# Optimization experiments

Measured on AMD Instinct MI355X. Metric: run time of the kernel, lower is better.

## Reference

```python
import jax, jax.numpy as jnp
import numpy as np

NG, N, NFG, NFR, NFP, B = 4, 64, 1024, 256, 256, 2048
SCALE = 1.0 / float(np.sqrt(NFR + NFP))
EPS = 1e-5  # torch LayerNorm default


def setup_inputs() -> dict:
    key = jax.random.key(0)
    k = jax.random.split(key, 4)
    x = jax.random.normal(k[0], (B, N, NFG), dtype=jnp.float32)
    # per-graph params stacked over NG for vectorized computation
    Wt = jax.random.normal(k[1], (NG, NFR, NFG), dtype=jnp.float32) * 0.02
    bt = jnp.zeros((NG, NFR), dtype=jnp.float32)
    Wp = jax.random.normal(k[2], (NG, NFR, NFG), dtype=jnp.float32) * 0.02
    bp = jnp.zeros((NG, NFR), dtype=jnp.float32)
    Wg = jax.random.normal(k[3], (NG, NFG, NFG), dtype=jnp.float32) * 0.02  # [out,in]
    gamma = jnp.ones((NG, NFG), dtype=jnp.float32)
    beta = jnp.zeros((NG, NFG), dtype=jnp.float32)
    return {"x": x, "Wt": Wt, "bt": bt, "Wp": Wp, "bp": bp,
            "Wg": Wg, "gamma": gamma, "beta": beta}


def reference(x, Wt, bt, Wp, bp, Wg, gamma, beta):
    # theta/phi projections, vectorized over NG graphs: [G,B,N,R]
    theta = jnp.einsum('bnf,grf->gbnr', x, Wt) + bt[:, None, None, :]
    phi = jnp.einsum('bnf,grf->gbnr', x, Wp) + bp[:, None, None, :]
    # original computes sim=theta@phi^T then .sum(2); identical math:
    # relation[b,n] = theta[b,n] . sum_m phi[b,m]  (avoids the NxN matrix)
    phi_sum = phi.sum(axis=2)                                  # [G,B,R]
    relation = jnp.einsum('gbnr,gbr->gbn', theta, phi_sum) * SCALE
    w = jax.nn.softmax(relation, axis=2)                       # softmax over boxes N
    # attention-weighted aggregation over boxes -> [G,B,NFG]
    agg = jnp.einsum('gbn,bnf->gbf', w, x)
    # GCN linear (no bias): [G,B,NFG]
    h = jnp.einsum('gbf,gof->gbo', agg, Wg)
    # LayerNorm over feature dim, per graph
    mu = h.mean(axis=-1, keepdims=True)
    var = ((h - mu) ** 2).mean(axis=-1, keepdims=True)
    h = (h - mu) * jax.lax.rsqrt(var + EPS) * gamma[:, None, :] + beta[:, None, :]
    h = jax.nn.relu(h)
    # mean over the NG graphs; restore keepdim axis -> [B,1,NFG]
    return h.mean(axis=0)[:, None, :]
```

## Files before the change

kernel.cpp:

```cpp
#include <hip/hip_runtime.h>
#include <hip/hip_bf16.h>

typedef __attribute__((ext_vector_type(4))) float f4;
typedef __attribute__((ext_vector_type(4))) float f32x4;
typedef __attribute__((ext_vector_type(8))) short short8;
typedef __attribute__((ext_vector_type(2))) unsigned int u32x2;
typedef __attribute__((ext_vector_type(4))) unsigned int u32x4;
typedef unsigned int u32;
typedef unsigned short u16;

#define SCALE_F 0.04419417382415922f

__device__ inline u16 f2bf(float f) {
  u32 u = __float_as_uint(f);
  u32 r = u + 0x7FFFu + ((u >> 16) & 1u);
  return (u16)(r >> 16);
}
__device__ inline u32 pk(float a, float b) {
  return (u32)f2bf(a) | ((u32)f2bf(b) << 16);
}
__device__ inline float bflo(u32 u) { return __uint_as_float(u << 16); }
__device__ inline float bfhi(u32 u) { return __uint_as_float(u & 0xFFFF0000u); }

#define GLD16(gsrc, ldst)                                                     \
  __builtin_amdgcn_global_load_lds(                                           \
      (const __attribute__((address_space(1))) void*)(gsrc),                  \
      (__attribute__((address_space(3))) void*)(ldst), 16, 0, 0)

#define SWZ(o) (((o) & ~2047) | (((((o) >> 4) & 127) ^ (((o) >> 11) & 7)) << 4))

__device__ __forceinline__ void cvt8(const float* __restrict__ src,
                                     u16* __restrict__ dst, int blk, int t) {
  int i = blk * 256 + t;
  const f4* s = (const f4*)src;
  f4 a = s[(size_t)i * 2];
  f4 b = s[(size_t)i * 2 + 1];
  u32x4 p;
  p[0] = pk(a[0], a[1]);
  p[1] = pk(a[2], a[3]);
  p[2] = pk(b[0], b[1]);
  p[3] = pk(b[2], b[3]);
  *(u32x4*)(dst + (size_t)i * 8) = p;
}

__global__ __launch_bounds__(256) void k01_prep(const float* __restrict__ x,
                                                const float* __restrict__ Wg,
                                                const float* __restrict__ Wp,
                                                const float* __restrict__ Wt,
                                                u16* __restrict__ xs16,
                                                char* __restrict__ xpre,
                                                u16* __restrict__ wgb,
                                                u16* __restrict__ wpb,
                                                u16* __restrict__ wtb) {
  __shared__ float red[256][8];
  __shared__ u16 tile[64][66];
  const int blk = blockIdx.x, t = threadIdx.x;
  if (blk < 2048) {
    const int b = blk;
    const float* xb = x + (size_t)b * 65536;
    char* xp = xpre + (size_t)b * 131072;
    const int g16 = t & 127, rp = t >> 7;
    f4 acc0 = {0.f, 0.f, 0.f, 0.f}, acc1 = {0.f, 0.f, 0.f, 0.f};
#pragma unroll 8
    for (int it = 0; it < 32; ++it) {
      int n = it * 2 + rp;
      const float* src = xb + n * 1024 + g16 * 8;
      f4 v0 = *(const f4*)(src);
      f4 v1 = *(const f4*)(src + 4);
      acc0 += v0;
      acc1 += v1;
      u32x4 p;
      p[0] = pk(v0[0], v0[1]);
      p[1] = pk(v0[2], v0[3]);
      p[2] = pk(v1[0], v1[1]);
      p[3] = pk(v1[2], v1[3]);
      *(u32x4*)(xp + n * 2048 + g16 * 16) = p;
    }
    *(f4*)&red[t][0] = acc0;
    *(f4*)&red[t][4] = acc1;
    __syncthreads();
    if (t < 128) {
      f4 s0 = *(const f4*)&red[t][0];
      f4 s1 = *(const f4*)&red[t][4];
      f4 q0 = *(const f4*)&red[t + 128][0];
      f4 q1 = *(const f4*)&red[t + 128][4];
      s0 += q0;
      s1 += q1;
      u32x4 p;
      p[0] = pk(s0[0], s0[1]);
      p[1] = pk(s0[2], s0[3]);
      p[2] = pk(s1[0], s1[1]);
      p[3] = pk(s1[2], s1[3]);
      *(u32x4*)(xs16 + (size_t)b * 1024 + t * 8) = p;
    }
  } else if (blk < 4096) {
    cvt8(Wg, wgb, blk - 2048, t);
  } else if (blk < 4608) {
    cvt8(Wp, wpb, blk - 4096, t);
  } else {
    const int bid = blk - 4608;
    const int g = bid >> 6, rem = bid & 63;
    const int f0 = (rem & 15) * 64, r0 = (rem >> 4) * 64;
    const float* src = Wt + ((size_t)g * 256 + r0) * 1024 + f0;
#pragma unroll
    for (int i = 0; i < 16; ++i) {
      int idx = t + i * 256;
      int rl = idx >> 6, fl = idx & 63;
      tile[fl][rl] = f2bf(src[rl * 1024 + fl]);
    }
    __syncthreads();
    u16* dst = wtb + ((size_t)g * 1024 + f0) * 256 + r0;
#pragma unroll
    for (int i = 0; i < 4; ++i) {
      int idx = t + i * 256;
      int fl = idx >> 4, rq = idx & 15;
      u32x2 p;
      p[0] = (u32)tile[fl][rq * 4]     | ((u32)tile[fl][rq * 4 + 1] << 16);
      p[1] = (u32)tile[fl][rq * 4 + 2] | ((u32)tile[fl][rq * 4 + 3] << 16);
      *(u32x2*)(dst + fl * 256 + rq * 4) = p;
    }
  }
}

__global__ __launch_bounds__(256) void k2_gemm(const u16* __restrict__ A,
                                               const u16* __restrict__ Bt,
                                               const float* __restrict__ bp,
                                               u16* __restrict__ C) {
  const int n0 = blockIdx.x * 64, m0 = blockIdx.y * 128;
  __shared__ u16 Al[128 * 32];
  __shared__ u16 Bl[64 * 32];
  const int t = threadIdx.x;
  const int w = t >> 6, l = t & 63;
  const int lr = l & 15, lh = l >> 4;
  f32x4 acc[2][4] = {};
  for (int kt = 0; kt < 1024; kt += 32) {
#pragma unroll
    for (int j = 0; j < 2; ++j) {
      int idx = t + j * 256;
      int row = idx >> 2, sl = idx & 3;
      GLD16(A + (size_t)(m0 + row) * 1024 + kt + sl * 8, Al + idx * 8);
    }
    {
      int row = t >> 2, sl = t & 3;
      GLD16(Bt + (size_t)(n0 + row) * 1024 + kt + sl * 8, Bl + t * 8);
    }
    __syncthreads();
    short8 af[2], bfr[4];
#pragma unroll
    for (int m = 0; m < 2; ++m)
      af[m] = *(const short8*)(Al + (w * 32 + m * 16 + lr) * 32 + lh * 8);
#pragma unroll
    for (int n = 0; n < 4; ++n)
      bfr[n] = *(const short8*)(Bl + (n * 16 + lr) * 32 + lh * 8);
#pragma unroll
    for (int m = 0; m < 2; ++m)
#pragma unroll
      for (int n = 0; n < 4; ++n)
        acc[m][n] = __builtin_amdgcn_mfma_f32_16x16x32_bf16(af[m], bfr[n],
                                                            acc[m][n], 0, 0, 0);
    __syncthreads();
  }
#pragma unroll
  for (int m = 0; m < 2; ++m)
#pragma unroll
    for (int n = 0; n < 4; ++n) {
      int col = n0 + n * 16 + lr;
      float bb = 64.0f * bp[col];
#pragma unroll
      for (int j = 0; j < 4; ++j)
        C[(size_t)(m0 + w * 32 + m * 16 + lh * 4 + j) * 1024 + col] =
            f2bf(acc[m][n][j] + bb);
    }
}

__global__ __launch_bounds__(256) void k3_gemm(const u16* __restrict__ A,
                                               const u16* __restrict__ Btt,
                                               u16* __restrict__ Vb) {
  const int g = blockIdx.z;
  const int n0 = blockIdx.x * 128, m0 = blockIdx.y * 128;
  const u16* Bg = Btt + (size_t)g * 1024 * 256;
  __shared__ u16 Al[128 * 32];
  __shared__ u16 Bl[128 * 32];
  const int t = threadIdx.x;
  const int w = t >> 6, l = t & 63;
  const int wr = w >> 1, wc = w & 1;
  const int lr = l & 15, lh = l >> 4;
  f32x4 acc[4][4] = {};
  for (int kt = 0; kt < 256; kt += 32) {
#pragma unroll
    for (int j = 0; j < 2; ++j) {
      int idx = t + j * 256;
      int row = idx >> 2, sl = idx & 3;
      GLD16(A + (size_t)(m0 + row) * 1024 + g * 256 + kt + sl * 8, Al + idx * 8);
      GLD16(Bg + (size_t)(n0 + row) * 256 + kt + sl * 8, Bl + idx * 8);
    }
    __syncthreads();
    short8 af[4], bfr[4];
#pragma unroll
    for (int m = 0; m < 4; ++m)
      af[m] = *(const short8*)(Al + (wr * 64 + m * 16 + lr) * 32 + lh * 8);
#pragma unroll
    for (int n = 0; n < 4; ++n)
      bfr[n] = *(const short8*)(Bl + (wc * 64 + n * 16 + lr) * 32 + lh * 8);
#pragma unroll
    for (int m = 0; m < 4; ++m)
#pragma unroll
      for (int n = 0; n < 4; ++n)
        acc[m][n] = __builtin_amdgcn_mfma_f32_16x16x32_bf16(af[m], bfr[n],
                                                            acc[m][n], 0, 0, 0);
    __syncthreads();
  }
  u16* Vg = Vb + (size_t)g * 2048 * 1024;
#pragma unroll
  for (int m = 0; m < 4; ++m)
#pragma unroll
    for (int n = 0; n < 4; ++n)
#pragma unroll
      for (int j = 0; j < 4; ++j)
        Vg[(size_t)(m0 + wr * 64 + m * 16 + lh * 4 + j) * 1024 +
           (n0 + wc * 64 + n * 16 + lr)] = f2bf(acc[m][n][j]);
}

__device__ __forceinline__ void relation_phase(const char* xl, const u16* vb,
                                               float* relp, int w, int l) {
  const int lg = l >> 4, lr = l & 15;
  f32x4 racc[4] = {};
#pragma unroll
  for (int kp = 0; kp < 2; ++kp) {
    const int kt = kp * 512 + w * 32;
    short8 afr = {};
    if (lr < 4) afr = *(const short8*)(vb + lr * 1032 + kt + lg * 8);
#pragma unroll
    for (int nt = 0; nt < 4; ++nt) {
      int n = nt * 16 + lr;
      short8 bfrg = *(const short8*)(
          xl + n * 2048 + ((((kt >> 3) + lg) ^ (n & 7)) << 4));
      racc[nt] = __builtin_amdgcn_mfma_f32_16x16x32_bf16(afr, bfrg, racc[nt],
                                                         0, 0, 0);
    }
  }
  if (l < 16) {
#pragma unroll
    for (int nt = 0; nt < 4; ++nt)
#pragma unroll
      for (int j = 0; j < 4; ++j)
        relp[(w * 4 + j) * 64 + nt * 16 + lr] = racc[nt][j];
  }
}

__device__ __forceinline__ void softmax_phase(const float* relp, float* wsm,
                                              int t) {
  if (t < 256) {
    const int g = t >> 6, n = t & 63;
    float rel = 0.f;
#pragma unroll
    for (int ww = 0; ww < 16; ++ww) rel += relp[(ww * 4 + g) * 64 + n];
    rel *= SCALE_F;
    float mx = rel;
#pragma unroll
    for (int o = 32; o > 0; o >>= 1) mx = fmaxf(mx, __shfl_xor(mx, o, 64));
    float e = __expf(rel - mx);
    float s = e;
#pragma unroll
    for (int o = 32; o > 0; o >>= 1) s += __shfl_xor(s, o, 64);
    wsm[t] = e / s;
  }
}

__device__ __forceinline__ void agg_phase(const char* xl, const float* wsm,
                                          float* relp, u16* aggb, int b,
                                          int t) {
  const int hh = t >> 9, r = t & 511, g = r >> 7, f8 = r & 127;
  const float* wg = wsm + g * 64 + hh * 32;
  float a0 = 0, a1 = 0, a2 = 0, a3 = 0, a4 = 0, a5 = 0, a6 = 0, a7 = 0;
#pragma unroll 8
  for (int n0 = 0; n0 < 32; ++n0) {
    int n = hh * 32 + n0;
    float wv = wg[n0];
    u32x4 xp = *(const u32x4*)(xl + n * 2048 + ((f8 ^ (n & 7)) << 4));
    a0 = fmaf(bflo(xp[0]), wv, a0);
    a1 = fmaf(bfhi(xp[0]), wv, a1);
    a2 = fmaf(bflo(xp[1]), wv, a2);
    a3 = fmaf(bfhi(xp[1]), wv, a3);
    a4 = fmaf(bflo(xp[2]), wv, a4);
    a5 = fmaf(bfhi(xp[2]), wv, a5);
    a6 = fmaf(bflo(xp[3]), wv, a6);
    a7 = fmaf(bfhi(xp[3]), wv, a7);
  }
  if (hh) {
    f4 q0 = {a0, a1, a2, a3};
    f4 q1 = {a4, a5, a6, a7};
    *(f4*)(relp + r * 8) = q0;
    *(f4*)(relp + r * 8 + 4) = q1;
  }
  __syncthreads();
  if (!hh) {
    f4 q0 = *(const f4*)(relp + r * 8);
    f4 q1 = *(const f4*)(relp + r * 8 + 4);
    u32x4 p;
    p[0] = pk(a0 + q0[0], a1 + q0[1]);
    p[1] = pk(a2 + q0[2], a3 + q0[3]);
    p[2] = pk(a4 + q1[0], a5 + q1[1]);
    p[3] = pk(a6 + q1[2], a7 + q1[3]);
    *(u32x4*)(aggb + ((size_t)g * 2048 + b) * 1024 + f8 * 8) = p;
  }
}

#define K4_LDS (131072 + 8256 + 16384 + 1024)
__global__ __launch_bounds__(1024) void k4_fused(const char* __restrict__ xpre,
                                                 const u16* __restrict__ vb16,
                                                 u16* __restrict__ aggb) {
  extern __shared__ char sm[];
  char* xl = sm;
  u16* vb = (u16*)(sm + 131072);
  float* relp = (float*)(sm + 131072 + 8256);
  float* wsm = (float*)(sm + 131072 + 8256 + 16384);
  const int t = threadIdx.x;
  const int w = t >> 6, l = t & 63;
  const int b0 = (1023 - blockIdx.x) * 2, b1 = b0 + 1;

  {
    int g = t >> 8, q = t & 255;
    u32x2 pv = *(const u32x2*)(vb16 + ((size_t)g * 2048 + b0) * 1024 + q * 4);
    *(u32x2*)(vb + g * 1032 + q * 4) = pv;
  }
  const char* xg0 = xpre + (size_t)b0 * 131072;
#pragma unroll
  for (int i = 0; i < 8; ++i) {
    int o = (w * 8 + i) * 1024 + l * 16;
    GLD16(xg0 + SWZ(o), xl + o);
  }
  __syncthreads();

  const char* xg1 = xpre + (size_t)b1 * 131072;
  u32x4 pf0 = *(const u32x4*)(xg1 + SWZ(t * 16));
  u32x4 pf1 = *(const u32x4*)(xg1 + SWZ(t * 16 + 16384));
  u32x4 pf2 = *(const u32x4*)(xg1 + SWZ(t * 16 + 32768));
  u32x4 pf3 = *(const u32x4*)(xg1 + SWZ(t * 16 + 49152));
  u32x4 pf4 = *(const u32x4*)(xg1 + SWZ(t * 16 + 65536));
  u32x4 pf5 = *(const u32x4*)(xg1 + SWZ(t * 16 + 81920));
  u32x4 pf6 = *(const u32x4*)(xg1 + SWZ(t * 16 + 98304));
  u32x4 pf7 = *(const u32x4*)(xg1 + SWZ(t * 16 + 114688));
  u32x2 pv1 =
      *(const u32x2*)(vb16 + ((size_t)(t >> 8) * 2048 + b1) * 1024 + (t & 255) * 4);

  relation_phase(xl, vb, relp, w, l);
  __syncthreads();
  softmax_phase(relp, wsm, t);
  __syncthreads();
  agg_phase(xl, wsm, relp, aggb, b0, t);
  __syncthreads();

  *(u32x4*)(xl + t * 16) = pf0;
  *(u32x4*)(xl + t * 16 + 16384) = pf1;
  *(u32x4*)(xl + t * 16 + 32768) = pf2;
  *(u32x4*)(xl + t * 16 + 49152) = pf3;
  *(u32x4*)(xl + t * 16 + 65536) = pf4;
  *(u32x4*)(xl + t * 16 + 81920) = pf5;
  *(u32x4*)(xl + t * 16 + 98304) = pf6;
  *(u32x4*)(xl + t * 16 + 114688) = pf7;
  {
    int g = t >> 8, q = t & 255;
    *(u32x2*)(vb + g * 1032 + q * 4) = pv1;
  }
  __syncthreads();

  relation_phase(xl, vb, relp, w, l);
  __syncthreads();
  softmax_phase(relp, wsm, t);
  __syncthreads();
  agg_phase(xl, wsm, relp, aggb, b1, t);
}

__global__ __launch_bounds__(256) void k5_gemm(const u16* __restrict__ Ab,
                                               const u16* __restrict__ Bb,
                                               u16* __restrict__ H) {
  const int g = blockIdx.z;
  const int n0 = blockIdx.x * 128, m0 = blockIdx.y * 128;
  const u16* A = Ab + (size_t)g * 2048 * 1024;
  const u16* Bt = Bb + (size_t)g * 1024 * 1024;
  __shared__ u16 Al[128 * 32];
  __shared__ u16 Bl[128 * 32];
  const int t = threadIdx.x;
  const int w = t >> 6, l = t & 63;
  const int wr = w >> 1, wc = w & 1;
  const int lr = l & 15, lh = l >> 4;
  f32x4 acc[4][4] = {};
  for (int kt = 0; kt < 1024; kt += 32) {
#pragma unroll
    for (int j = 0; j < 2; ++j) {
      int idx = t + j * 256;
      int row = idx >> 2, sl = idx & 3;
      GLD16(A + (size_t)(m0 + row) * 1024 + kt + sl * 8, Al + idx * 8);
      GLD16(Bt + (size_t)(n0 + row) * 1024 + kt + sl * 8, Bl + idx * 8);
    }
    __syncthreads();
    short8 af[4], bfr[4];
#pragma unroll
    for (int m = 0; m < 4; ++m)
      af[m] = *(const short8*)(Al + (wr * 64 + m * 16 + lr) * 32 + lh * 8);
#pragma unroll
    for (int n = 0; n < 4; ++n)
      bfr[n] = *(const short8*)(Bl + (wc * 64 + n * 16 + lr) * 32 + lh * 8);
#pragma unroll
    for (int m = 0; m < 4; ++m)
#pragma unroll
      for (int n = 0; n < 4; ++n)
        acc[m][n] = __builtin_amdgcn_mfma_f32_16x16x32_bf16(af[m], bfr[n],
                                                            acc[m][n], 0, 0, 0);
    __syncthreads();
  }
  u16* Hg = H + (size_t)g * 2048 * 1024;
#pragma unroll
  for (int m = 0; m < 4; ++m)
#pragma unroll
    for (int n = 0; n < 4; ++n)
#pragma unroll
      for (int j = 0; j < 4; ++j)
        Hg[(size_t)(m0 + wr * 64 + m * 16 + lh * 4 + j) * 1024 +
           (n0 + wc * 64 + n * 16 + lr)] = f2bf(acc[m][n][j]);
}

__global__ __launch_bounds__(256) void k6_ln(const u16* __restrict__ H,
                                             const float* __restrict__ gamma,
                                             const float* __restrict__ beta,
                                             float* __restrict__ out) {
  const int b = blockIdx.x, t = threadIdx.x;
  const int w = t >> 6, lane = t & 63;
  __shared__ float red[8];
  f4 acc = {0.f, 0.f, 0.f, 0.f};
  for (int g = 0; g < 4; ++g) {
    u32x2 hp = *(const u32x2*)(H + ((size_t)g * 2048 + b) * 1024 + t * 4);
    f4 hv = {bflo(hp[0]), bfhi(hp[0]), bflo(hp[1]), bfhi(hp[1])};
    float s = hv[0] + hv[1] + hv[2] + hv[3];
    float q = hv[0] * hv[0] + hv[1] * hv[1] + hv[2] * hv[2] + hv[3] * hv[3];
#pragma unroll
    for (int o = 32; o > 0; o >>= 1) {
      s += __shfl_xor(s, o, 64);
      q += __shfl_xor(q, o, 64);
    }
    if (lane == 0) { red[w] = s; red[4 + w] = q; }
    __syncthreads();
    s = red[0] + red[1] + red[2] + red[3];
    q = red[4] + red[5] + red[6] + red[7];
    float mean = s * (1.f / 1024.f);
    float var = q * (1.f / 1024.f) - mean * mean;
    float rstd = rsqrtf(var + 1e-5f);
    f4 gm = *(const f4*)(gamma + g * 1024 + t * 4);
    f4 bt = *(const f4*)(beta + g * 1024 + t * 4);
#pragma unroll
    for (int j = 0; j < 4; ++j) {
      float val = (hv[j] - mean) * rstd * gm[j] + bt[j];
      acc[j] += fmaxf(val, 0.f);
    }
    __syncthreads();
  }
  acc *= 0.25f;
  *(f4*)(out + (size_t)b * 1024 + t * 4) = acc;
}

extern "C" void kernel_launch(void* const* d_in, const int* in_sizes, int n_in,
                              void* d_out, int out_size, void* d_ws, size_t ws_size,
                              hipStream_t stream) {
  const float* x     = (const float*)d_in[0];
  const float* Wt    = (const float*)d_in[1];
  const float* Wp    = (const float*)d_in[3];
  const float* bp    = (const float*)d_in[4];
  const float* Wg    = (const float*)d_in[5];
  const float* gamma = (const float*)d_in[6];
  const float* beta  = (const float*)d_in[7];
  float* out = (float*)d_out;

  char* ws = (char*)d_ws;
  u16*   xs16 = (u16*)(ws);
  u16*   ps16 = (u16*)(ws + (4u << 20));
  u16*   wpb  = (u16*)(ws + (8u << 20));
  u16*   wtb  = (u16*)(ws + (10u << 20));
  u16*   wgb  = (u16*)(ws + (12u << 20));
  u16*   vb16 = (u16*)(ws + (20u << 20));
  u16*   aggb = (u16*)(ws + (36u << 20));
  u16*   hb16 = (u16*)(ws + (52u << 20));
  char*  xpre = (char*)(ws + (68u << 20));

  hipFuncSetAttribute((const void*)k4_fused,
                      hipFuncAttributeMaxDynamicSharedMemorySize, K4_LDS);

  k01_prep<<<4864, 256, 0, stream>>>(x, Wg, Wp, Wt, xs16, xpre, wgb, wpb, wtb);
  k2_gemm<<<dim3(16, 16), 256, 0, stream>>>(xs16, wpb, bp, ps16);
  k3_gemm<<<dim3(8, 16, 4), 256, 0, stream>>>(ps16, wtb, vb16);
  k4_fused<<<1024, 1024, K4_LDS, stream>>>(xpre, vb16, aggb);
  k5_gemm<<<dim3(8, 16, 4), 256, 0, stream>>>(aggb, wgb, hb16);
  k6_ln<<<2048, 256, 0, stream>>>(hb16, gamma, beta, out);
}
```

Before: 329.3 us.

## Process eight batches per k4 block and remap GEMM block ids for XCD locality

The fused relation/softmax/aggregation kernel now loops over eight consecutive batch items per block instead of two, prefetching the next item's x tile and v vector into registers while the current one is computed. The grid drops to 256 blocks, exactly one per CU on MI355X. The k3 and k5 GEMMs switch to a 1D grid with a block-id permutation so that blocks sharing operands land on the same XCD and can reuse L2. The trade-off is fewer blocks in flight for k4 and longer serial chains per block, with no tail overlap.

```diff
diff --git a/kernel.cpp b/kernel.cpp
--- a/kernel.cpp
+++ b/kernel.cpp
@@ -176,8 +176,9 @@
 __global__ __launch_bounds__(256) void k3_gemm(const u16* __restrict__ A,
                                                const u16* __restrict__ Btt,
                                                u16* __restrict__ Vb) {
-  const int g = blockIdx.z;
-  const int n0 = blockIdx.x * 128, m0 = blockIdx.y * 128;
+  const int id = blockIdx.x;
+  const int wg = (id & 7) * 64 + (id >> 3);
+  const int n0 = (wg & 7) * 128, m0 = ((wg >> 3) & 15) * 128, g = wg >> 7;
   const u16* Bg = Btt + (size_t)g * 1024 * 256;
   __shared__ u16 Al[128 * 32];
   __shared__ u16 Bl[128 * 32];
@@ -317,14 +318,14 @@
   float* wsm = (float*)(sm + 131072 + 8256 + 16384);
   const int t = threadIdx.x;
   const int w = t >> 6, l = t & 63;
-  const int b0 = (1023 - blockIdx.x) * 2, b1 = b0 + 1;
+  const int bbase = (255 - (int)blockIdx.x) * 8;
 
   {
     int g = t >> 8, q = t & 255;
-    u32x2 pv = *(const u32x2*)(vb16 + ((size_t)g * 2048 + b0) * 1024 + q * 4);
+    u32x2 pv = *(const u32x2*)(vb16 + ((size_t)g * 2048 + bbase) * 1024 + q * 4);
     *(u32x2*)(vb + g * 1032 + q * 4) = pv;
   }
-  const char* xg0 = xpre + (size_t)b0 * 131072;
+  const char* xg0 = xpre + (size_t)bbase * 131072;
 #pragma unroll
   for (int i = 0; i < 8; ++i) {
     int o = (w * 8 + i) * 1024 + l * 16;
@@ -332,51 +333,50 @@
   }
   __syncthreads();
 
-  const char* xg1 = xpre + (size_t)b1 * 131072;
-  u32x4 pf0 = *(const u32x4*)(xg1 + SWZ(t * 16));
-  u32x4 pf1 = *(const u32x4*)(xg1 + SWZ(t * 16 + 16384));
-  u32x4 pf2 = *(const u32x4*)(xg1 + SWZ(t * 16 + 32768));
-  u32x4 pf3 = *(const u32x4*)(xg1 + SWZ(t * 16 + 49152));
-  u32x4 pf4 = *(const u32x4*)(xg1 + SWZ(t * 16 + 65536));
-  u32x4 pf5 = *(const u32x4*)(xg1 + SWZ(t * 16 + 81920));
-  u32x4 pf6 = *(const u32x4*)(xg1 + SWZ(t * 16 + 98304));
-  u32x4 pf7 = *(const u32x4*)(xg1 + SWZ(t * 16 + 114688));
-  u32x2 pv1 =
-      *(const u32x2*)(vb16 + ((size_t)(t >> 8) * 2048 + b1) * 1024 + (t & 255) * 4);
-
-  relation_phase(xl, vb, relp, w, l);
-  __syncthreads();
-  softmax_phase(relp, wsm, t);
-  __syncthreads();
-  agg_phase(xl, wsm, relp, aggb, b0, t);
-  __syncthreads();
-
-  *(u32x4*)(xl + t * 16) = pf0;
-  *(u32x4*)(xl + t * 16 + 16384) = pf1;
-  *(u32x4*)(xl + t * 16 + 32768) = pf2;
-  *(u32x4*)(xl + t * 16 + 49152) = pf3;
-  *(u32x4*)(xl + t * 16 + 65536) = pf4;
-  *(u32x4*)(xl + t * 16 + 81920) = pf5;
-  *(u32x4*)(xl + t * 16 + 98304) = pf6;
-  *(u32x4*)(xl + t * 16 + 114688) = pf7;
-  {
-    int g = t >> 8, q = t & 255;
-    *(u32x2*)(vb + g * 1032 + q * 4) = pv1;
-  }
-  __syncthreads();
-
-  relation_phase(xl, vb, relp, w, l);
-  __syncthreads();
-  softmax_phase(relp, wsm, t);
-  __syncthreads();
-  agg_phase(xl, wsm, relp, aggb, b1, t);
+  u32x4 pf0, pf1, pf2, pf3, pf4, pf5, pf6, pf7;
+  u32x2 pv1;
+  for (int ib = 0; ib < 8; ++ib) {
+    const int b = bbase + ib;
+    if (ib < 7) {
+      const char* xg1 = xpre + (size_t)(b + 1) * 131072;
+      pf0 = *(const u32x4*)(xg1 + SWZ(t * 16));
+      pf1 = *(const u32x4*)(xg1 + SWZ(t * 16 + 16384));
+      pf2 = *(const u32x4*)(xg1 + SWZ(t * 16 + 32768));
+      pf3 = *(const u32x4*)(xg1 + SWZ(t * 16 + 49152));
+      pf4 = *(const u32x4*)(xg1 + SWZ(t * 16 + 65536));
+      pf5 = *(const u32x4*)(xg1 + SWZ(t * 16 + 81920));
+      pf6 = *(const u32x4*)(xg1 + SWZ(t * 16 + 98304));
+      pf7 = *(const u32x4*)(xg1 + SWZ(t * 16 + 114688));
+      pv1 = *(const u32x2*)(vb16 + ((size_t)(t >> 8) * 2048 + (b + 1)) * 1024 +
+                            (t & 255) * 4);
+    }
+    relation_phase(xl, vb, relp, w, l);
+    __syncthreads();
+    softmax_phase(relp, wsm, t);
+    __syncthreads();
+    agg_phase(xl, wsm, relp, aggb, b, t);
+    __syncthreads();
+    if (ib < 7) {
+      *(u32x4*)(xl + t * 16) = pf0;
+      *(u32x4*)(xl + t * 16 + 16384) = pf1;
+      *(u32x4*)(xl + t * 16 + 32768) = pf2;
+      *(u32x4*)(xl + t * 16 + 49152) = pf3;
+      *(u32x4*)(xl + t * 16 + 65536) = pf4;
+      *(u32x4*)(xl + t * 16 + 81920) = pf5;
+      *(u32x4*)(xl + t * 16 + 98304) = pf6;
+      *(u32x4*)(xl + t * 16 + 114688) = pf7;
+      *(u32x2*)(vb + (t >> 8) * 1032 + (t & 255) * 4) = pv1;
+      __syncthreads();
+    }
+  }
 }
 
 __global__ __launch_bounds__(256) void k5_gemm(const u16* __restrict__ Ab,
                                                const u16* __restrict__ Bb,
                                                u16* __restrict__ H) {
-  const int g = blockIdx.z;
-  const int n0 = blockIdx.x * 128, m0 = blockIdx.y * 128;
+  const int id = blockIdx.x;
+  const int wg = (id & 7) * 64 + (id >> 3);
+  const int n0 = (wg & 7) * 128, m0 = ((wg >> 3) & 15) * 128, g = wg >> 7;
   const u16* A = Ab + (size_t)g * 2048 * 1024;
   const u16* Bt = Bb + (size_t)g * 1024 * 1024;
   __shared__ u16 Al[128 * 32];
@@ -487,8 +487,8 @@
 
   k01_prep<<<4864, 256, 0, stream>>>(x, Wg, Wp, Wt, xs16, xpre, wgb, wpb, wtb);
   k2_gemm<<<dim3(16, 16), 256, 0, stream>>>(xs16, wpb, bp, ps16);
-  k3_gemm<<<dim3(8, 16, 4), 256, 0, stream>>>(ps16, wtb, vb16);
-  k4_fused<<<1024, 1024, K4_LDS, stream>>>(xpre, vb16, aggb);
-  k5_gemm<<<dim3(8, 16, 4), 256, 0, stream>>>(aggb, wgb, hb16);
+  k3_gemm<<<512, 256, 0, stream>>>(ps16, wtb, vb16);
+  k4_fused<<<256, 1024, K4_LDS, stream>>>(xpre, vb16, aggb);
+  k5_gemm<<<512, 256, 0, stream>>>(aggb, wgb, hb16);
   k6_ln<<<2048, 256, 0, stream>>>(hb16, gamma, beta, out);
 }
```

Measured after the change: 311.5 us. 5.4% less time.
